# Kernel optimization log

Hardware: AMD Instinct MI355X
Metric: run time of the kernel (lower is better)

## Reference

```python
import jax, jax.numpy as jnp
import numpy as np

NUM_SEQS = 64
NUM_HEADS = 32
NUM_KV_HEADS = 8
HEAD_SIZE = 128
BLOCK_SIZE = 16
X = 8  # vector packing factor of the key cache
MAX_BLOCKS_PER_SEQ = 128  # max_context_len 2048 / block_size 16
NUM_BLOCKS = 8192
SCALE = 0.08838834764831845  # 1/sqrt(128)
NEG_INF = -1e30


def setup_inputs() -> dict:
    key = jax.random.key(0)
    k1, k2, k3, k4, k5 = jax.random.split(key, 5)
    query = jax.random.normal(k1, (NUM_SEQS, NUM_HEADS, HEAD_SIZE), dtype=jnp.float32)
    key_cache = jax.random.normal(
        k2, (NUM_BLOCKS, NUM_KV_HEADS, HEAD_SIZE // X, BLOCK_SIZE, X), dtype=jnp.float32)
    value_cache = jax.random.normal(
        k3, (NUM_BLOCKS, NUM_KV_HEADS, HEAD_SIZE, BLOCK_SIZE), dtype=jnp.float32)
    block_tables = jax.random.randint(
        k4, (NUM_SEQS, MAX_BLOCKS_PER_SEQ), 0, NUM_BLOCKS, dtype=jnp.int32)
    # context lengths in [1024, 2048] so no sequence is empty
    context_lens = jax.random.randint(k5, (NUM_SEQS,), 1024, 2049, dtype=jnp.int32)
    return {"query": query, "key_cache": key_cache, "value_cache": value_cache,
            "block_tables": block_tables, "context_lens": context_lens}


def _paged_attention(query, key_cache, value_cache, block_tables, context_lens):
    s, nh, hs = query.shape
    nb = block_tables.shape[1]
    kvh = key_cache.shape[1]
    bs = value_cache.shape[3]
    qpk = nh // kvh  # queries per kv head (GQA)
    T = nb * bs      # max context length (padded)

    # Gather K blocks: [s, nb, kvh, hs/x, bs, x] -> [s, T, kvh, hs]
    k = key_cache[block_tables]
    k = jnp.transpose(k, (0, 1, 4, 2, 3, 5)).reshape(s, T, kvh, hs)
    # Gather V blocks: [s, nb, kvh, hs, bs] -> [s, T, kvh, hs]
    v = value_cache[block_tables]
    v = jnp.transpose(v, (0, 1, 4, 2, 3)).reshape(s, T, kvh, hs)

    q = query.reshape(s, kvh, qpk, hs)
    scores = jnp.einsum('sgqd,stgd->sgqt', q, k) * SCALE  # [s, kvh, qpk, T]
    valid = (jnp.arange(T, dtype=jnp.int32)[None, :] < context_lens[:, None])  # [s, T]
    scores = jnp.where(valid[:, None, None, :], scores, NEG_INF)
    w = jax.nn.softmax(scores, axis=-1)
    out = jnp.einsum('sgqt,stgd->sgqd', w, v)  # [s, kvh, qpk, hs]
    return out.reshape(s, nh * hs)


def reference(query, key_cache, value_cache, block_tables, context_lens):
    return _paged_attention(query, key_cache, value_cache, block_tables, context_lens)
```

## Files before the change

kernel.cpp:

```cpp
#include <hip/hip_runtime.h>
#include <hip/hip_bf16.h>

#define NSEQ 64
#define NH 32
#define KVH 8
#define QPK 4
#define HS 128
#define BS 16
#define MAXB 128
#define KVBLK 2048
#define SCALE 0.08838834764831845f

__device__ __forceinline__ float bflo(unsigned int u) { return __uint_as_float(u << 16); }
__device__ __forceinline__ float bfhi(unsigned int u) { return __uint_as_float(u & 0xffff0000u); }

template<bool ISBF>
__device__ __forceinline__ void load8(const void* base, long long eoff, float* o) {
    if constexpr (ISBF) {
        const uint4 u = *(const uint4*)((const unsigned short*)base + eoff);
        o[0] = bflo(u.x); o[1] = bfhi(u.x);
        o[2] = bflo(u.y); o[3] = bfhi(u.y);
        o[4] = bflo(u.z); o[5] = bfhi(u.z);
        o[6] = bflo(u.w); o[7] = bfhi(u.w);
    } else {
        const float4* p = (const float4*)((const float*)base + eoff);
        const float4 a = p[0]; const float4 b = p[1];
        o[0] = a.x; o[1] = a.y; o[2] = a.z; o[3] = a.w;
        o[4] = b.x; o[5] = b.y; o[6] = b.z; o[7] = b.w;
    }
}

__device__ __forceinline__ bool detect_bf16(const void* q) {
    const int lane = threadIdx.x & 63;
    int bad = 0;
    const unsigned int* qu = (const unsigned int*)q;
    #pragma unroll
    for (int i = 0; i < 4; ++i) {
        const unsigned int u = qu[lane * 4 + i];
        const float lo = bflo(u), hi = bfhi(u);
        if (!(__builtin_fabsf(lo) <= 64.f) || !(__builtin_fabsf(hi) <= 64.f)) bad = 1;
    }
    return (__ballot(bad) == 0ull);
}

template<bool ISBF>
__device__ __forceinline__ void attn_split_body(
    const void* __restrict__ qp, const void* __restrict__ kp, const void* __restrict__ vp,
    const int* __restrict__ bt, const int* __restrict__ cl,
    float* __restrict__ accws, float* __restrict__ lws, void* __restrict__ outp)
{
    const int g    = blockIdx.x;
    const int s    = blockIdx.y;
    const int z    = blockIdx.z;
    const int nsp  = gridDim.z;
    const int tid  = threadIdx.x;
    const int wave = tid >> 6;
    const int lane = tid & 63;
    const int h    = g * QPK + wave;
    const int t    = lane & 15;
    const int c4   = lane >> 4;
    const int drow = lane >> 1;
    const int half = lane & 1;

    __shared__ __align__(16) float w_lds[4][BS];

    const int ctx = cl[s];
    const int nblocks = (ctx + BS - 1) >> 4;
    const int bpx = (nblocks + nsp - 1) / nsp;
    const int bstart = z * bpx;
    const int bend = min(bstart + bpx, nblocks);

    float qreg[4][8];
    {
        const long long qbase = (long long)(s * NH + h) * HS;
        #pragma unroll
        for (int cc = 0; cc < 4; ++cc) {
            load8<ISBF>(qp, qbase + (4 * c4 + cc) * 8, qreg[cc]);
            #pragma unroll
            for (int x = 0; x < 8; ++x) qreg[cc][x] *= SCALE;
        }
    }

    float l_run = 0.f;
    float acc[4] = {0.f, 0.f, 0.f, 0.f};

    if (bstart < bend) {
        const int* btrow = bt + s * MAXB;
        long long pb_next = btrow[bstart];
        for (int b = bstart; b < bend; ++b) {
            const long long pb = pb_next;
            pb_next = btrow[(b + 1 < bend) ? b + 1 : b];
            const long long kvb = (pb * KVH + g) * KVBLK;

            float kvals[4][8];
            #pragma unroll
            for (int cc = 0; cc < 4; ++cc)
                load8<ISBF>(kp, kvb + ((4 * c4 + cc) * 16 + t) * 8, kvals[cc]);

            float s0 = 0.f, s1 = 0.f;
            #pragma unroll
            for (int x = 0; x < 8; ++x) {
                s0 = fmaf(qreg[0][x], kvals[0][x], s0);
                s1 = fmaf(qreg[1][x], kvals[1][x], s1);
            }
            #pragma unroll
            for (int x = 0; x < 8; ++x) {
                s0 = fmaf(qreg[2][x], kvals[2][x], s0);
                s1 = fmaf(qreg[3][x], kvals[3][x], s1);
            }
            float sc = s0 + s1;
            sc += __shfl_xor(sc, 16);
            sc += __shfl_xor(sc, 32);

            const int tok = b * BS + t;
            const float p = (tok < ctx) ? __expf(sc) : 0.f;
            l_run += p;

            if (lane < 16) w_lds[wave][t] = p;
            float wreg[8];
            {
                const float4* wp = (const float4*)&w_lds[wave][half * 8];
                const float4 w0 = wp[0]; const float4 w1 = wp[1];
                wreg[0] = w0.x; wreg[1] = w0.y; wreg[2] = w0.z; wreg[3] = w0.w;
                wreg[4] = w1.x; wreg[5] = w1.y; wreg[6] = w1.z; wreg[7] = w1.w;
            }

            #pragma unroll
            for (int j = 0; j < 4; ++j) {
                float vvals[8];
                load8<ISBF>(vp, kvb + (long long)((drow + 32 * j) * 16 + half * 8), vvals);
                float a0 = acc[j];
                #pragma unroll
                for (int k = 0; k < 8; ++k) a0 = fmaf(wreg[k], vvals[k], a0);
                acc[j] = a0;
            }
        }
    }

    #pragma unroll
    for (int j = 0; j < 4; ++j) acc[j] += __shfl_xor(acc[j], 1);

    float l = l_run;
    l += __shfl_xor(l, 1);
    l += __shfl_xor(l, 2);
    l += __shfl_xor(l, 4);
    l += __shfl_xor(l, 8);
    l += __shfl_xor(l, 16);
    l += __shfl_xor(l, 32);
    l *= 0.25f;

    if (nsp == 1) {
        const float inv = 1.f / l;
        if (half == 0) {
            const long long ob = (long long)(s * NH + h) * HS;
            #pragma unroll
            for (int j = 0; j < 4; ++j) {
                const float o = acc[j] * inv;
                const long long oi = ob + drow + 32 * j;
                if constexpr (ISBF) ((__hip_bfloat16*)outp)[oi] = __float2bfloat16(o);
                else                ((float*)outp)[oi] = o;
            }
        }
    } else {
        const long long base = ((long long)z * NSEQ + s) * NH + h;
        if (half == 0) {
            #pragma unroll
            for (int j = 0; j < 4; ++j)
                accws[base * HS + drow + 32 * j] = acc[j];
        }
        if (lane == 0) lws[base] = l;
    }
}

__global__ __launch_bounds__(256, 4) void PagedAttention_69312182223772_kernel(
    const void* __restrict__ q, const void* __restrict__ k, const void* __restrict__ v,
    const int* __restrict__ bt, const int* __restrict__ cl,
    float* __restrict__ accws, float* __restrict__ lws, void* __restrict__ out)
{
    const bool isbf = detect_bf16(q);
    if (isbf) attn_split_body<true >(q, k, v, bt, cl, accws, lws, out);
    else      attn_split_body<false>(q, k, v, bt, cl, accws, lws, out);
}

__global__ __launch_bounds__(128) void PagedAttention_combine_kernel(
    const void* __restrict__ q, const float* __restrict__ accws,
    const float* __restrict__ lws, void* __restrict__ out, int nsp)
{
    const bool isbf = detect_bf16(q);
    const int hh = blockIdx.x;
    const int s  = blockIdx.y;
    const int d  = threadIdx.x;
    float num = 0.f, den = 0.f;
    for (int zz = 0; zz < nsp; ++zz) {
        const long long base = ((long long)zz * NSEQ + s) * NH + hh;
        den += lws[base];
        num += accws[base * HS + d];
    }
    const float o = num / den;
    const long long oi = (long long)(s * NH + hh) * HS + d;
    if (isbf) ((__hip_bfloat16*)out)[oi] = __float2bfloat16(o);
    else      ((float*)out)[oi] = o;
}

extern "C" void kernel_launch(void* const* d_in, const int* in_sizes, int n_in,
                              void* d_out, int out_size, void* d_ws, size_t ws_size,
                              hipStream_t stream) {
    const void* q  = d_in[0];
    const void* kc = d_in[1];
    const void* vc = d_in[2];
    const int* bt  = (const int*)d_in[3];
    const int* cl  = (const int*)d_in[4];

    auto need = [](int S) -> size_t {
        return (size_t)S * NSEQ * NH * (HS + 1) * sizeof(float);
    };
    int S = 1;
    if (ws_size >= need(4)) S = 4;
    else if (ws_size >= need(2)) S = 2;

    float* accws = (float*)d_ws;
    float* lws   = accws + (size_t)S * NSEQ * NH * HS;

    dim3 grid(KVH, NSEQ, S);
    PagedAttention_69312182223772_kernel<<<grid, 256, 0, stream>>>(
        q, kc, vc, bt, cl, accws, lws, d_out);

    if (S > 1) {
        dim3 cgrid(NH, NSEQ);
        PagedAttention_combine_kernel<<<cgrid, 128, 0, stream>>>(
            q, accws, lws, d_out, S);
    }
}
```

Measured before the change: 977.7 us.

## Share KV loads across GQA heads, split blocks across waves, prefetch K

Each wave now handles all four query heads of a KV group and strides over KV blocks with the other waves, so every K/V block is loaded once per workgroup instead of once per head. Partial results from the four waves are reduced through LDS before the split output is written. The next K block is prefetched while the current one is computed. Scaling folds in log2e so exp2 can be used. The split count drops from 4 to 2 and launch bounds are relaxed. The cost is much higher register pressure from four heads' q and acc values, lower occupancy, and an extra LDS reduction step.

Result: faster. 924.0 us (-5.5%).

```diff
diff --git a/kernel.cpp b/kernel.cpp
--- a/kernel.cpp
+++ b/kernel.cpp
@@ -10,6 +10,7 @@
 #define MAXB 128
 #define KVBLK 2048
 #define SCALE 0.08838834764831845f
+#define LOG2E 1.4426950408889634f
 
 __device__ __forceinline__ float bflo(unsigned int u) { return __uint_as_float(u << 16); }
 __device__ __forceinline__ float bfhi(unsigned int u) { return __uint_as_float(u & 0xffff0000u); }
@@ -44,7 +45,7 @@
 }
 
 template<bool ISBF>
-__device__ __forceinline__ void attn_split_body(
+__device__ __forceinline__ void attn_body(
     const void* __restrict__ qp, const void* __restrict__ kp, const void* __restrict__ vp,
     const int* __restrict__ bt, const int* __restrict__ cl,
     float* __restrict__ accws, float* __restrict__ lws, void* __restrict__ outp)
@@ -56,13 +57,14 @@
     const int tid  = threadIdx.x;
     const int wave = tid >> 6;
     const int lane = tid & 63;
-    const int h    = g * QPK + wave;
     const int t    = lane & 15;
     const int c4   = lane >> 4;
     const int drow = lane >> 1;
     const int half = lane & 1;
 
-    __shared__ __align__(16) float w_lds[4][BS];
+    __shared__ __align__(16) float w_lds[4][QPK][BS];
+    __shared__ float l_lds[4][QPK];
+    __shared__ float acc_lds[4][QPK][HS];
 
     const int ctx = cl[s];
     const int nblocks = (ctx + BS - 1) >> 4;
@@ -70,116 +72,163 @@
     const int bstart = z * bpx;
     const int bend = min(bstart + bpx, nblocks);
 
-    float qreg[4][8];
+    float qreg[QPK][4][8];
     {
-        const long long qbase = (long long)(s * NH + h) * HS;
-        #pragma unroll
-        for (int cc = 0; cc < 4; ++cc) {
-            load8<ISBF>(qp, qbase + (4 * c4 + cc) * 8, qreg[cc]);
-            #pragma unroll
-            for (int x = 0; x < 8; ++x) qreg[cc][x] *= SCALE;
-        }
-    }
-
-    float l_run = 0.f;
-    float acc[4] = {0.f, 0.f, 0.f, 0.f};
-
-    if (bstart < bend) {
-        const int* btrow = bt + s * MAXB;
-        long long pb_next = btrow[bstart];
-        for (int b = bstart; b < bend; ++b) {
-            const long long pb = pb_next;
-            pb_next = btrow[(b + 1 < bend) ? b + 1 : b];
-            const long long kvb = (pb * KVH + g) * KVBLK;
-
-            float kvals[4][8];
-            #pragma unroll
-            for (int cc = 0; cc < 4; ++cc)
-                load8<ISBF>(kp, kvb + ((4 * c4 + cc) * 16 + t) * 8, kvals[cc]);
-
+        const long long qbase = (long long)(s * NH + g * QPK) * HS;
+        #pragma unroll
+        for (int h = 0; h < QPK; ++h)
+            #pragma unroll
+            for (int cc = 0; cc < 4; ++cc) {
+                load8<ISBF>(qp, qbase + h * HS + (4 * c4 + cc) * 8, qreg[h][cc]);
+                #pragma unroll
+                for (int x = 0; x < 8; ++x) qreg[h][cc][x] *= SCALE * LOG2E;
+            }
+    }
+
+    float l_run[QPK] = {0.f, 0.f, 0.f, 0.f};
+    float acc[QPK][4];
+    #pragma unroll
+    for (int h = 0; h < QPK; ++h)
+        #pragma unroll
+        for (int j = 0; j < 4; ++j) acc[h][j] = 0.f;
+
+    const int* btrow = bt + s * MAXB;
+    int b = bstart + wave;
+
+    float kv[4][8];
+    long long kvb = 0;
+    if (b < bend) {
+        kvb = ((long long)btrow[b] * KVH + g) * KVBLK;
+        #pragma unroll
+        for (int cc = 0; cc < 4; ++cc)
+            load8<ISBF>(kp, kvb + ((4 * c4 + cc) * 16 + t) * 8, kv[cc]);
+    }
+
+    for (; b < bend; b += 4) {
+        float vv[4][8];
+        #pragma unroll
+        for (int j = 0; j < 4; ++j)
+            load8<ISBF>(vp, kvb + (long long)((drow + 32 * j) * 16 + half * 8), vv[j]);
+
+        float sc[QPK];
+        #pragma unroll
+        for (int h = 0; h < QPK; ++h) {
             float s0 = 0.f, s1 = 0.f;
             #pragma unroll
             for (int x = 0; x < 8; ++x) {
-                s0 = fmaf(qreg[0][x], kvals[0][x], s0);
-                s1 = fmaf(qreg[1][x], kvals[1][x], s1);
+                s0 = fmaf(qreg[h][0][x], kv[0][x], s0);
+                s1 = fmaf(qreg[h][1][x], kv[1][x], s1);
             }
             #pragma unroll
             for (int x = 0; x < 8; ++x) {
-                s0 = fmaf(qreg[2][x], kvals[2][x], s0);
-                s1 = fmaf(qreg[3][x], kvals[3][x], s1);
-            }
-            float sc = s0 + s1;
-            sc += __shfl_xor(sc, 16);
-            sc += __shfl_xor(sc, 32);
-
-            const int tok = b * BS + t;
-            const float p = (tok < ctx) ? __expf(sc) : 0.f;
-            l_run += p;
-
-            if (lane < 16) w_lds[wave][t] = p;
+                s0 = fmaf(qreg[h][2][x], kv[2][x], s0);
+                s1 = fmaf(qreg[h][3][x], kv[3][x], s1);
+            }
+            sc[h] = s0 + s1;
+        }
+
+        const int bn = (b + 4 < bend) ? (b + 4) : b;
+        const long long kvbn = ((long long)btrow[bn] * KVH + g) * KVBLK;
+        #pragma unroll
+        for (int cc = 0; cc < 4; ++cc)
+            load8<ISBF>(kp, kvbn + ((4 * cc / 4 * 4 + cc) * 0 + (4 * c4 + cc) * 16 + t) * 8, kv[cc]);
+
+        #pragma unroll
+        for (int h = 0; h < QPK; ++h) {
+            sc[h] += __shfl_xor(sc[h], 16);
+            sc[h] += __shfl_xor(sc[h], 32);
+        }
+
+        const int tok = b * BS + t;
+        float p[QPK];
+        #pragma unroll
+        for (int h = 0; h < QPK; ++h) {
+            p[h] = (tok < ctx) ? __builtin_amdgcn_exp2f(sc[h]) : 0.f;
+            l_run[h] += p[h];
+        }
+
+        if (lane < 16) {
+            #pragma unroll
+            for (int h = 0; h < QPK; ++h) w_lds[wave][h][t] = p[h];
+        }
+
+        #pragma unroll
+        for (int h = 0; h < QPK; ++h) {
+            const float4* wp = (const float4*)&w_lds[wave][h][half * 8];
+            const float4 w0 = wp[0]; const float4 w1 = wp[1];
             float wreg[8];
-            {
-                const float4* wp = (const float4*)&w_lds[wave][half * 8];
-                const float4 w0 = wp[0]; const float4 w1 = wp[1];
-                wreg[0] = w0.x; wreg[1] = w0.y; wreg[2] = w0.z; wreg[3] = w0.w;
-                wreg[4] = w1.x; wreg[5] = w1.y; wreg[6] = w1.z; wreg[7] = w1.w;
-            }
-
+            wreg[0] = w0.x; wreg[1] = w0.y; wreg[2] = w0.z; wreg[3] = w0.w;
+            wreg[4] = w1.x; wreg[5] = w1.y; wreg[6] = w1.z; wreg[7] = w1.w;
             #pragma unroll
             for (int j = 0; j < 4; ++j) {
-                float vvals[8];
-                load8<ISBF>(vp, kvb + (long long)((drow + 32 * j) * 16 + half * 8), vvals);
-                float a0 = acc[j];
+                float a0 = acc[h][j];
                 #pragma unroll
-                for (int k = 0; k < 8; ++k) a0 = fmaf(wreg[k], vvals[k], a0);
-                acc[j] = a0;
-            }
-        }
-    }
-
-    #pragma unroll
-    for (int j = 0; j < 4; ++j) acc[j] += __shfl_xor(acc[j], 1);
-
-    float l = l_run;
-    l += __shfl_xor(l, 1);
-    l += __shfl_xor(l, 2);
-    l += __shfl_xor(l, 4);
-    l += __shfl_xor(l, 8);
-    l += __shfl_xor(l, 16);
-    l += __shfl_xor(l, 32);
-    l *= 0.25f;
-
-    if (nsp == 1) {
-        const float inv = 1.f / l;
-        if (half == 0) {
-            const long long ob = (long long)(s * NH + h) * HS;
-            #pragma unroll
-            for (int j = 0; j < 4; ++j) {
-                const float o = acc[j] * inv;
-                const long long oi = ob + drow + 32 * j;
-                if constexpr (ISBF) ((__hip_bfloat16*)outp)[oi] = __float2bfloat16(o);
-                else                ((float*)outp)[oi] = o;
-            }
-        }
-    } else {
-        const long long base = ((long long)z * NSEQ + s) * NH + h;
-        if (half == 0) {
+                for (int k = 0; k < 8; ++k) a0 = fmaf(wreg[k], vv[j][k], a0);
+                acc[h][j] = a0;
+            }
+        }
+
+        kvb = kvbn;
+    }
+
+    #pragma unroll
+    for (int h = 0; h < QPK; ++h)
+        #pragma unroll
+        for (int j = 0; j < 4; ++j)
+            acc[h][j] += __shfl_xor(acc[h][j], 1);
+
+    #pragma unroll
+    for (int h = 0; h < QPK; ++h) {
+        float l = l_run[h];
+        l += __shfl_xor(l, 1);
+        l += __shfl_xor(l, 2);
+        l += __shfl_xor(l, 4);
+        l += __shfl_xor(l, 8);
+        l += __shfl_xor(l, 16);
+        l += __shfl_xor(l, 32);
+        l_run[h] = l * 0.25f;
+    }
+
+    if (half == 0) {
+        #pragma unroll
+        for (int h = 0; h < QPK; ++h)
             #pragma unroll
             for (int j = 0; j < 4; ++j)
-                accws[base * HS + drow + 32 * j] = acc[j];
-        }
-        if (lane == 0) lws[base] = l;
-    }
-}
-
-__global__ __launch_bounds__(256, 4) void PagedAttention_69312182223772_kernel(
+                acc_lds[wave][h][drow + 32 * j] = acc[h][j];
+    }
+    if (lane == 0) {
+        #pragma unroll
+        for (int h = 0; h < QPK; ++h) l_lds[wave][h] = l_run[h];
+    }
+    __syncthreads();
+
+    for (int i = tid; i < QPK * HS; i += 256) {
+        const int h = i >> 7;
+        const int d = i & (HS - 1);
+        const float den = l_lds[0][h] + l_lds[1][h] + l_lds[2][h] + l_lds[3][h];
+        const float val = acc_lds[0][h][d] + acc_lds[1][h][d]
+                        + acc_lds[2][h][d] + acc_lds[3][h][d];
+        if (nsp == 1) {
+            const float o = val / den;
+            const long long oi = (long long)s * (NH * HS) + (long long)(g * QPK + h) * HS + d;
+            if constexpr (ISBF) ((__hip_bfloat16*)outp)[oi] = __float2bfloat16(o);
+            else                ((float*)outp)[oi] = o;
+        } else {
+            const long long base = ((long long)z * NSEQ + s) * NH + (g * QPK + h);
+            accws[base * HS + d] = val;
+            if (d == 0) lws[base] = den;
+        }
+    }
+}
+
+__global__ __launch_bounds__(256, 2) void PagedAttention_69312182223772_kernel(
     const void* __restrict__ q, const void* __restrict__ k, const void* __restrict__ v,
     const int* __restrict__ bt, const int* __restrict__ cl,
     float* __restrict__ accws, float* __restrict__ lws, void* __restrict__ out)
 {
     const bool isbf = detect_bf16(q);
-    if (isbf) attn_split_body<true >(q, k, v, bt, cl, accws, lws, out);
-    else      attn_split_body<false>(q, k, v, bt, cl, accws, lws, out);
+    if (isbf) attn_body<true >(q, k, v, bt, cl, accws, lws, out);
+    else      attn_body<false>(q, k, v, bt, cl, accws, lws, out);
 }
 
 __global__ __launch_bounds__(128) void PagedAttention_combine_kernel(
@@ -214,9 +263,7 @@
     auto need = [](int S) -> size_t {
         return (size_t)S * NSEQ * NH * (HS + 1) * sizeof(float);
     };
-    int S = 1;
-    if (ws_size >= need(4)) S = 4;
-    else if (ws_size >= need(2)) S = 2;
+    int S = (ws_size >= need(2)) ? 2 : 1;
 
     float* accws = (float*)d_ws;
     float* lws   = accws + (size_t)S * NSEQ * NH * HS;
```
